# Optimization experiments

Measured on AMD Instinct MI355X. Metric: run time of the kernel, lower is better.

## Reference

```python
import jax, jax.numpy as jnp
import numpy as np

N, E, F, R, L = 20000, 320000, 128, 20, 3
CUTOFF = 5.0
EPS = 1e-15


def _p(k, shape, fan_in):
    return jax.random.normal(k, shape, dtype=jnp.float32) * (fan_in ** -0.5)


def setup_inputs() -> dict:
    key = jax.random.key(0)
    ks = jax.random.split(key, 30)
    xyz = jax.random.uniform(ks[0], (N, 3), dtype=jnp.float32, minval=0.0, maxval=12.0)
    z = jax.random.randint(ks[1], (N,), 1, 84)
    i = jax.random.randint(ks[2], (E,), 0, N)
    off = jax.random.randint(ks[3], (E,), 1, N)
    j = (i + off) % N  # guarantees i != j
    nbrs = jnp.stack([i, j], axis=1)
    return {
        'xyz': xyz, 'z': z, 'nbrs': nbrs,
        'embed': _p(ks[4], (100, F), 1),
        'msg_W1': _p(ks[5], (L, F, F), F), 'msg_b1': jnp.zeros((L, F)),
        'msg_W2': _p(ks[6], (L, F, 3 * F), F), 'msg_b2': jnp.zeros((L, 3 * F)),
        'msg_Wd': _p(ks[7], (L, R, 3 * F), R), 'msg_bd': jnp.zeros((L, 3 * F)),
        'upd_U': _p(ks[8], (L, F, F), F), 'upd_V': _p(ks[9], (L, F, F), F),
        'upd_Ws1': _p(ks[10], (L, 2 * F, F), 2 * F), 'upd_bs1': jnp.zeros((L, F)),
        'upd_Ws2': _p(ks[11], (L, F, 3 * F), F), 'upd_bs2': jnp.zeros((L, 3 * F)),
        'ro_W1': _p(ks[12], (F, F // 2), F), 'ro_b1': jnp.zeros((F // 2,)),
        'ro_W2': _p(ks[13], (F // 2, 64), F // 2), 'ro_b2': jnp.zeros((64,)),
        'fc_W1': _p(ks[14], (64, 128), 64), 'fc_b1': jnp.zeros((128,)),
        'fc_W2': _p(ks[15], (128, 128), 128), 'fc_b2': jnp.zeros((128,)),
        'fc_Wo': _p(ks[16], (128, 1), 128), 'fc_bo': jnp.zeros((1,)),
    }


def _painn_forward(xyz, z, nbrs, embed,
                   msg_W1, msg_b1, msg_W2, msg_b2, msg_Wd, msg_bd,
                   upd_U, upd_V, upd_Ws1, upd_bs1, upd_Ws2, upd_bs2,
                   ro_W1, ro_b1, ro_W2, ro_b2,
                   fc_W1, fc_b1, fc_W2, fc_b2, fc_Wo, fc_bo):
    n_atoms = xyz.shape[0]
    idx_i, idx_j = nbrs[:, 0], nbrs[:, 1]
    # neighbor displacement vectors, distances, unit vectors
    r_ij = xyz[idx_j] - xyz[idx_i]                       # [E,3]
    dist = jnp.sqrt(jnp.sum(r_ij * r_ij, -1) + EPS)      # [E]
    unit = r_ij / dist[:, None]                          # [E,3]
    # PaiNN radial basis: sin(n*pi*d/cutoff)/d, n=1..R
    n_k = jnp.arange(1, R + 1, dtype=xyz.dtype)
    rbf = jnp.sin(n_k * jnp.pi * dist[:, None] / CUTOFF) / dist[:, None]   # [E,R]
    f_cut = jnp.where(dist < CUTOFF, 0.5 * (jnp.cos(jnp.pi * dist / CUTOFF) + 1.0), 0.0)
    silu = jax.nn.silu
    s = embed[z]                                         # [N,F]
    v = jnp.zeros((n_atoms, F, 3), dtype=xyz.dtype)      # [N,F,3]
    for l in range(L):
        # --- message block ---
        phi = silu(s @ msg_W1[l] + msg_b1[l]) @ msg_W2[l] + msg_b2[l]      # [N,3F]
        w_s = (rbf @ msg_Wd[l] + msg_bd[l]) * f_cut[:, None]               # [E,3F]
        inv = (phi[idx_j] * w_s).reshape(-1, 3, F)                         # [E,3,F]
        s0, s1, s2 = inv[:, 0], inv[:, 1], inv[:, 2]
        dv_ij = s2[:, :, None] * unit[:, None, :] + s0[:, :, None] * v[idx_j]  # [E,F,3]
        ds_i = jax.ops.segment_sum(s1, idx_i, num_segments=n_atoms)
        dv_i = jax.ops.segment_sum(dv_ij, idx_i, num_segments=n_atoms)
        s = s + ds_i
        v = v + dv_i
        # --- update block ---
        u_v = jnp.einsum('nfd,fg->ngd', v, upd_U[l])
        v_v = jnp.einsum('nfd,fg->ngd', v, upd_V[l])
        v_norm = jnp.sqrt(jnp.sum(v_v * v_v, -1) + EPS)                    # [N,F]
        stack = jnp.concatenate([s, v_norm], axis=-1)                      # [N,2F]
        split = silu(stack @ upd_Ws1[l] + upd_bs1[l]) @ upd_Ws2[l] + upd_bs2[l]
        a_vv = split[:, :F, None]
        a_sv = split[:, F:2 * F]
        a_ss = split[:, 2 * F:]
        v = v + u_v * a_vv
        s = s + jnp.sum(u_v * v_v, -1) * a_sv + a_ss
    # --- readout + fully connected head (per atom) ---
    h = silu(s @ ro_W1 + ro_b1) @ ro_W2 + ro_b2                            # [N,64]
    h = jax.nn.relu(h @ fc_W1 + fc_b1)
    h = jax.nn.relu(h @ fc_W2 + fc_b2)
    return h @ fc_Wo + fc_bo                                               # [N,1]


def reference(xyz, z, nbrs, embed,
              msg_W1, msg_b1, msg_W2, msg_b2, msg_Wd, msg_bd,
              upd_U, upd_V, upd_Ws1, upd_bs1, upd_Ws2, upd_bs2,
              ro_W1, ro_b1, ro_W2, ro_b2,
              fc_W1, fc_b1, fc_W2, fc_b2, fc_Wo, fc_bo):
    return _painn_forward(xyz, z, nbrs, embed,
                          msg_W1, msg_b1, msg_W2, msg_b2, msg_Wd, msg_bd,
                          upd_U, upd_V, upd_Ws1, upd_bs1, upd_Ws2, upd_bs2,
                          ro_W1, ro_b1, ro_W2, ro_b2,
                          fc_W1, fc_b1, fc_W2, fc_b2, fc_Wo, fc_bo)
```

## Files before the change

kernel.cpp:

```cpp
#include <hip/hip_runtime.h>
#include <math.h>

static const int NA = 20000;
static const int NE = 320000;
static const int F  = 128;
static const long NF = (long)NA * F;

typedef short short8 __attribute__((ext_vector_type(8)));
typedef float f32x4  __attribute__((ext_vector_type(4)));

__global__ void geom_kernel(const float* __restrict__ xyz, const int* __restrict__ nbrs,
                            float* __restrict__ edata, int* __restrict__ act,
                            int* __restrict__ cnt) {
    int e = blockIdx.x * 256 + threadIdx.x;
    if (e >= NE) return;
    int i = nbrs[2 * e], j = nbrs[2 * e + 1];
    float xi = xyz[3 * i], yi = xyz[3 * i + 1], zi = xyz[3 * i + 2];
    float xj = xyz[3 * j], yj = xyz[3 * j + 1], zj = xyz[3 * j + 2];
    float rx = xj - xi, ry = yj - yi, rz = zj - zi;
    float d2 = rx * rx + ry * ry + rz * rz + 1e-15f;
    float d = sqrtf(d2);
    if (d >= 5.0f) { act[e] = 0; return; }
    act[e] = 1;
    atomicAdd(&cnt[i], 1);
    float inv = 1.0f / d;
    float fc = 0.5f * (cosf(d * (float)M_PI / 5.0f) + 1.0f);
    float* ed = edata + (size_t)e * 24;
    ed[0] = fc; ed[1] = rx * inv; ed[2] = ry * inv; ed[3] = rz * inv;
    float x = d * (float)M_PI / 5.0f;
    float s1 = sinf(x), c1 = cosf(x);
    float skm1 = 0.f, sk = s1;
    float twoc = 2.f * c1;
    float scale = inv * fc;
    #pragma unroll
    for (int k = 0; k < 20; k++) {
        ed[4 + k] = sk * scale;
        float skp1 = twoc * sk - skm1;
        skm1 = sk; sk = skp1;
    }
}

__global__ __launch_bounds__(1024) void scan_kernel(const int* __restrict__ cnt, int* __restrict__ offs) {
    __shared__ int sh[1024];
    const int CH = 20;
    int t = threadIdx.x;
    int base = t * CH;
    int c[CH];
    int tot = 0;
    #pragma unroll
    for (int k = 0; k < CH; k++) {
        int idx = base + k;
        c[k] = (idx < NA) ? cnt[idx] : 0;
        tot += c[k];
    }
    sh[t] = tot;
    __syncthreads();
    for (int o = 1; o < 1024; o <<= 1) {
        int v = (t >= o) ? sh[t - o] : 0;
        __syncthreads();
        sh[t] += v;
        __syncthreads();
    }
    int run = sh[t] - tot;
    #pragma unroll
    for (int k = 0; k < CH; k++) {
        int idx = base + k;
        if (idx < NA) offs[idx] = run;
        run += c[k];
    }
    if (t == 1023) offs[NA] = sh[1023];
}

__global__ void fill_kernel(const int* __restrict__ nbrs, const int* __restrict__ act,
                            const int* __restrict__ offs, int* __restrict__ cur,
                            const float* __restrict__ edata,
                            int* __restrict__ jc, float* __restrict__ edc) {
    int e = blockIdx.x * 256 + threadIdx.x;
    if (e >= NE || !act[e]) return;
    int i = nbrs[2 * e];
    int q = offs[i] + atomicAdd(&cur[i], 1);
    jc[q] = nbrs[2 * e + 1];
    const float4* src = (const float4*)(edata + (size_t)e * 24);
    float4* dst = (float4*)(edc + (size_t)q * 24);
    #pragma unroll
    for (int k = 0; k < 6; k++) dst[k] = src[k];
}

__global__ void embed_kernel(const int* __restrict__ z, const float* __restrict__ embed,
                             float* __restrict__ s, __bf16* __restrict__ sh_, __bf16* __restrict__ sl_) {
    int idx = blockIdx.x * 256 + threadIdx.x;
    if (idx >= NA * F) return;
    int n = idx >> 7, f = idx & 127;
    float v = embed[z[n] * F + f];
    s[idx] = v;
    __bf16 h = (__bf16)v;
    sh_[idx] = h; sl_[idx] = (__bf16)(v - (float)h);
}

static const int WSEG = 180224;
static const int WRO  = 3 * WSEG;
static const int WTOT = WRO + 36864;

__global__ void wconv_kernel(const float* __restrict__ W1, const float* __restrict__ W2,
                             const float* __restrict__ U, const float* __restrict__ V,
                             const float* __restrict__ Ws1, const float* __restrict__ Ws2,
                             const float* __restrict__ roW1, const float* __restrict__ roW2,
                             const float* __restrict__ fcW1, const float* __restrict__ fcW2,
                             __bf16* __restrict__ wh, __bf16* __restrict__ wl) {
    int g = blockIdx.x * 256 + threadIdx.x;
    if (g >= WTOT) return;
    const float* src; int K, N, idx;
    if (g < WRO) {
        int lay = g / WSEG, o = g - lay * WSEG;
        if (o < 16384)       { src = W1  + (size_t)lay * 16384; K = 128; N = 128; idx = o; }
        else if (o < 65536)  { src = W2  + (size_t)lay * 49152; K = 128; N = 384; idx = o - 16384; }
        else if (o < 81920)  { src = U   + (size_t)lay * 16384; K = 128; N = 128; idx = o - 65536; }
        else if (o < 98304)  { src = V   + (size_t)lay * 16384; K = 128; N = 128; idx = o - 81920; }
        else if (o < 131072) { src = Ws1 + (size_t)lay * 32768; K = 256; N = 128; idx = o - 98304; }
        else                 { src = Ws2 + (size_t)lay * 49152; K = 128; N = 384; idx = o - 131072; }
    } else {
        int o2 = g - WRO;
        if (o2 < 8192)       { src = roW1; K = 128; N = 64;  idx = o2; }
        else if (o2 < 12288) { src = roW2; K = 64;  N = 64;  idx = o2 - 8192; }
        else if (o2 < 20480) { src = fcW1; K = 64;  N = 128; idx = o2 - 12288; }
        else                 { src = fcW2; K = 128; N = 128; idx = o2 - 20480; }
    }
    int n = idx / K, k = idx - n * K;
    float v = src[(size_t)k * N + n];
    __bf16 h = (__bf16)v;
    wh[g] = h; wl[g] = (__bf16)(v - (float)h);
}

template<int ACT, int MODE>
__device__ __forceinline__ void mgemm_body(char* ldsb,
    const __bf16* __restrict__ Ah, const __bf16* __restrict__ Al,
    const __bf16* __restrict__ Bh, const __bf16* __restrict__ Bl,
    const float* __restrict__ bias, int K, int N, int c0,
    float* __restrict__ Cf, __bf16* __restrict__ Ch, __bf16* __restrict__ Cl) {
    int tid = threadIdx.x;
    int w = tid >> 6, l = tid & 63;
    int r0 = blockIdx.x * 128;

    int srow = tid >> 3, sl = tid & 7;

    int wr = w >> 2, wc = w & 3;
    int lrow = l & 15, lk = l >> 4;
    uint32_t arow[4], axor[4], brow[2], bxor[2];
    #pragma unroll
    for (int m = 0; m < 4; m++) {
        int row = wr * 64 + m * 16 + lrow;
        arow[m] = (uint32_t)row * 128u; axor[m] = (uint32_t)((row & 7) << 4);
    }
    #pragma unroll
    for (int n = 0; n < 2; n++) {
        int row = wc * 32 + n * 16 + lrow;
        brow[n] = (uint32_t)row * 128u; bxor[n] = (uint32_t)((row & 7) << 4);
    }

    f32x4 acc[4][2];
    #pragma unroll
    for (int m = 0; m < 4; m++)
        #pragma unroll
        for (int n = 0; n < 2; n++) acc[m][n] = (f32x4){0.f, 0.f, 0.f, 0.f};

    const char* pAh = (const char*)Ah;
    const char* pAl = (const char*)Al;
    const char* pBh = (const char*)Bh;
    const char* pBl = (const char*)Bl;

    for (int k0 = 0; k0 < K; k0 += 64) {
        #pragma unroll
        for (int t = 0; t < 2; t++) {
            int row = srow + t * 64;
            uint32_t dst = (uint32_t)row * 128u + (uint32_t)(((sl ^ (row & 7)) << 4));
            int ga = min(r0 + row, NA - 1);
            int gb = min(c0 + row, N - 1);
            size_t soA = ((size_t)ga * K + k0 + sl * 8) * 2;
            size_t soB = ((size_t)gb * K + k0 + sl * 8) * 2;
            *(float4*)(ldsb + dst)         = *(const float4*)(pAh + soA);
            *(float4*)(ldsb + 16384 + dst) = *(const float4*)(pAl + soA);
            *(float4*)(ldsb + 32768 + dst) = *(const float4*)(pBh + soB);
            *(float4*)(ldsb + 49152 + dst) = *(const float4*)(pBl + soB);
        }
        __syncthreads();
        #pragma unroll
        for (int kh = 0; kh < 2; kh++) {
            uint32_t ks = (uint32_t)((kh * 4 + lk) * 16);
            short8 fah[4], fal[4], fbh[2], fbl[2];
            #pragma unroll
            for (int m = 0; m < 4; m++) {
                uint32_t ob = arow[m] + (ks ^ axor[m]);
                fah[m] = *(const short8*)(ldsb + ob);
                fal[m] = *(const short8*)(ldsb + 16384 + ob);
            }
            #pragma unroll
            for (int n = 0; n < 2; n++) {
                uint32_t ob = brow[n] + (ks ^ bxor[n]);
                fbh[n] = *(const short8*)(ldsb + 32768 + ob);
                fbl[n] = *(const short8*)(ldsb + 49152 + ob);
            }
            #pragma unroll
            for (int m = 0; m < 4; m++)
                #pragma unroll
                for (int n = 0; n < 2; n++) {
                    acc[m][n] = __builtin_amdgcn_mfma_f32_16x16x32_bf16(fah[m], fbh[n], acc[m][n], 0, 0, 0);
                    acc[m][n] = __builtin_amdgcn_mfma_f32_16x16x32_bf16(fah[m], fbl[n], acc[m][n], 0, 0, 0);
                    acc[m][n] = __builtin_amdgcn_mfma_f32_16x16x32_bf16(fal[m], fbh[n], acc[m][n], 0, 0, 0);
                }
        }
        __syncthreads();
    }

    #pragma unroll
    for (int n = 0; n < 2; n++) {
        int gc = c0 + wc * 32 + n * 16 + lrow;
        float bb = (bias && gc < N) ? bias[gc] : 0.f;
        #pragma unroll
        for (int m = 0; m < 4; m++) {
            #pragma unroll
            for (int r = 0; r < 4; r++) {
                int gr = r0 + wr * 64 + m * 16 + lk * 4 + r;
                if (gr < NA && gc < N) {
                    float y = acc[m][n][r] + bb;
                    if (ACT == 1) y = y / (1.f + expf(-y));
                    if (ACT == 2) y = fmaxf(y, 0.f);
                    if (MODE == 0) {
                        Cf[(size_t)gr * N + gc] = y;
                    } else {
                        __bf16 h = (__bf16)y;
                        Ch[(size_t)gr * N + gc] = h;
                        Cl[(size_t)gr * N + gc] = (__bf16)(y - (float)h);
                    }
                }
            }
        }
    }
}

template<int ACT, int MODE>
__global__ __launch_bounds__(512, 4) void mgemm_kernel(
    const __bf16* __restrict__ Ah, const __bf16* __restrict__ Al,
    const __bf16* __restrict__ Bh, const __bf16* __restrict__ Bl,
    const float* __restrict__ bias, int K, int N,
    float* __restrict__ Cf, __bf16* __restrict__ Ch, __bf16* __restrict__ Cl) {
    __shared__ __attribute__((aligned(16))) char lds[65536];
    mgemm_body<ACT, MODE>(lds, Ah, Al, Bh, Bl, bias, K, N, blockIdx.y * 128, Cf, Ch, Cl);
}

__global__ __launch_bounds__(512, 4) void mgemm_uvvv_kernel(
    const __bf16* __restrict__ vBh, const __bf16* __restrict__ vBl,
    const __bf16* __restrict__ Uth, const __bf16* __restrict__ Utl,
    const __bf16* __restrict__ Vth, const __bf16* __restrict__ Vtl,
    float* __restrict__ uv, float* __restrict__ vv) {
    __shared__ __attribute__((aligned(16))) char lds[65536];
    int zz = blockIdx.z, d = zz % 3;
    const __bf16* Ah = vBh + (size_t)d * NF;
    const __bf16* Al = vBl + (size_t)d * NF;
    const __bf16* Bh = (zz < 3) ? Uth : Vth;
    const __bf16* Bl = (zz < 3) ? Utl : Vtl;
    float* Cf = ((zz < 3) ? uv : vv) + (size_t)d * NF;
    mgemm_body<0, 0>(lds, Ah, Al, Bh, Bl, nullptr, 128, 128, 0, Cf, nullptr, nullptr);
}

__global__ __launch_bounds__(512, 4) void mgemm_ws1_kernel(
    const __bf16* __restrict__ sh_, const __bf16* __restrict__ sl_,
    const float* __restrict__ vv,
    const __bf16* __restrict__ Bh, const __bf16* __restrict__ Bl,
    const float* __restrict__ bias,
    __bf16* __restrict__ Ch, __bf16* __restrict__ Cl) {
    __shared__ __attribute__((aligned(16))) char ldsb[65536];
    const int K = 256, N = 128;
    int tid = threadIdx.x;
    int w = tid >> 6, l = tid & 63;
    int r0 = blockIdx.x * 128;
    int srow = tid >> 3, sl = tid & 7;
    int wr = w >> 2, wc = w & 3;
    int lrow = l & 15, lk = l >> 4;
    uint32_t arow[4], axor[4], brow[2], bxor[2];
    #pragma unroll
    for (int m = 0; m < 4; m++) {
        int row = wr * 64 + m * 16 + lrow;
        arow[m] = (uint32_t)row * 128u; axor[m] = (uint32_t)((row & 7) << 4);
    }
    #pragma unroll
    for (int n = 0; n < 2; n++) {
        int row = wc * 32 + n * 16 + lrow;
        brow[n] = (uint32_t)row * 128u; bxor[n] = (uint32_t)((row & 7) << 4);
    }
    f32x4 acc[4][2];
    #pragma unroll
    for (int m = 0; m < 4; m++)
        #pragma unroll
        for (int n = 0; n < 2; n++) acc[m][n] = (f32x4){0.f, 0.f, 0.f, 0.f};

    for (int k0 = 0; k0 < K; k0 += 64) {
        #pragma unroll
        for (int t = 0; t < 2; t++) {
            int row = srow + t * 64;
            uint32_t dst = (uint32_t)row * 128u + (uint32_t)(((sl ^ (row & 7)) << 4));
            int ga = min(r0 + row, NA - 1);
            int gb = row;
            size_t soB = ((size_t)gb * K + k0 + sl * 8) * 2;
            *(float4*)(ldsb + 32768 + dst) = *(const float4*)((const char*)Bh + soB);
            *(float4*)(ldsb + 49152 + dst) = *(const float4*)((const char*)Bl + soB);
            if (k0 < 128) {
                size_t soA = ((size_t)ga * 128 + k0 + sl * 8) * 2;
                *(float4*)(ldsb + dst)         = *(const float4*)((const char*)sh_ + soA);
                *(float4*)(ldsb + 16384 + dst) = *(const float4*)((const char*)sl_ + soA);
            } else {
                int f0 = (k0 - 128) + sl * 8;
                size_t b = (size_t)ga * 128 + f0;
                float4 a0 = *(const float4*)(vv + b);
                float4 a1 = *(const float4*)(vv + b + 4);
                float4 b0 = *(const float4*)(vv + NF + b);
                float4 b1 = *(const float4*)(vv + NF + b + 4);
                float4 c0v = *(const float4*)(vv + 2 * NF + b);
                float4 c1v = *(const float4*)(vv + 2 * NF + b + 4);
                float xs[8] = {a0.x, a0.y, a0.z, a0.w, a1.x, a1.y, a1.z, a1.w};
                float ys[8] = {b0.x, b0.y, b0.z, b0.w, b1.x, b1.y, b1.z, b1.w};
                float zs[8] = {c0v.x, c0v.y, c0v.z, c0v.w, c1v.x, c1v.y, c1v.z, c1v.w};
                union { short8 s; float4 q; } hi, lo;
                #pragma unroll
                for (int k = 0; k < 8; k++) {
                    float vn = sqrtf(xs[k] * xs[k] + ys[k] * ys[k] + zs[k] * zs[k] + 1e-15f);
                    __bf16 h = (__bf16)vn;
                    hi.s[k] = *(short*)&h;
                    __bf16 lo_b = (__bf16)(vn - (float)h);
                    lo.s[k] = *(short*)&lo_b;
                }
                *(float4*)(ldsb + dst)         = hi.q;
                *(float4*)(ldsb + 16384 + dst) = lo.q;
            }
        }
        __syncthreads();
        #pragma unroll
        for (int kh = 0; kh < 2; kh++) {
            uint32_t ks = (uint32_t)((kh * 4 + lk) * 16);
            short8 fah[4], fal[4], fbh[2], fbl[2];
            #pragma unroll
            for (int m = 0; m < 4; m++) {
                uint32_t ob = arow[m] + (ks ^ axor[m]);
                fah[m] = *(const short8*)(ldsb + ob);
                fal[m] = *(const short8*)(ldsb + 16384 + ob);
            }
            #pragma unroll
            for (int n = 0; n < 2; n++) {
                uint32_t ob = brow[n] + (ks ^ bxor[n]);
                fbh[n] = *(const short8*)(ldsb + 32768 + ob);
                fbl[n] = *(const short8*)(ldsb + 49152 + ob);
            }
            #pragma unroll
            for (int m = 0; m < 4; m++)
                #pragma unroll
                for (int n = 0; n < 2; n++) {
                    acc[m][n] = __builtin_amdgcn_mfma_f32_16x16x32_bf16(fah[m], fbh[n], acc[m][n], 0, 0, 0);
                    acc[m][n] = __builtin_amdgcn_mfma_f32_16x16x32_bf16(fah[m], fbl[n], acc[m][n], 0, 0, 0);
                    acc[m][n] = __builtin_amdgcn_mfma_f32_16x16x32_bf16(fal[m], fbh[n], acc[m][n], 0, 0, 0);
                }
        }
        __syncthreads();
    }
    #pragma unroll
    for (int n = 0; n < 2; n++) {
        int gc = wc * 32 + n * 16 + lrow;
        float bb = bias[gc];
        #pragma unroll
        for (int m = 0; m < 4; m++) {
            #pragma unroll
            for (int r = 0; r < 4; r++) {
                int gr = r0 + wr * 64 + m * 16 + lk * 4 + r;
                if (gr < NA) {
                    float y = acc[m][n][r] + bb;
                    y = y / (1.f + expf(-y));
                    __bf16 h = (__bf16)y;
                    Ch[(size_t)gr * N + gc] = h;
                    Cl[(size_t)gr * N + gc] = (__bf16)(y - (float)h);
                }
            }
        }
    }
}

__global__ __launch_bounds__(128) void msg_kernel(
    const float* __restrict__ phi, const float* __restrict__ edc,
    const int* __restrict__ jc, const int* __restrict__ offs,
    const float* __restrict__ Wd, const float* __restrict__ bd,
    const float* __restrict__ vin, float* __restrict__ s,
    __bf16* __restrict__ sh_, __bf16* __restrict__ sl_,
    __bf16* __restrict__ vBh, __bf16* __restrict__ vBl) {
    int i = blockIdx.x;
    int f = threadIdx.x;
    float wd0[20], wd1[20], wd2[20];
    #pragma unroll
    for (int k = 0; k < 20; k++) {
        wd0[k] = Wd[k * 384 + f];
        wd1[k] = Wd[k * 384 + 128 + f];
        wd2[k] = Wd[k * 384 + 256 + f];
    }
    float b0 = bd[f], b1 = bd[128 + f], b2 = bd[256 + f];
    float accS = 0.f, aV0 = 0.f, aV1 = 0.f, aV2 = 0.f;
    int p0 = offs[i], p1 = offs[i + 1];
    for (int p = p0; p < p1; ++p) {
        int j = jc[p];
        const float4* ed = (const float4*)(edc + (size_t)p * 24);
        float4 q0 = ed[0], q1 = ed[1], q2 = ed[2], q3 = ed[3], q4 = ed[4], q5 = ed[5];
        float fc = q0.x, ux = q0.y, uy = q0.z, uz = q0.w;
        float rb[20];
        rb[0]=q1.x; rb[1]=q1.y; rb[2]=q1.z; rb[3]=q1.w;
        rb[4]=q2.x; rb[5]=q2.y; rb[6]=q2.z; rb[7]=q2.w;
        rb[8]=q3.x; rb[9]=q3.y; rb[10]=q3.z; rb[11]=q3.w;
        rb[12]=q4.x; rb[13]=q4.y; rb[14]=q4.z; rb[15]=q4.w;
        rb[16]=q5.x; rb[17]=q5.y; rb[18]=q5.z; rb[19]=q5.w;
        float w0 = b0 * fc, w1 = b1 * fc, w2 = b2 * fc;
        #pragma unroll
        for (int k = 0; k < 20; k++) {
            w0 += rb[k] * wd0[k];
            w1 += rb[k] * wd1[k];
            w2 += rb[k] * wd2[k];
        }
        const float* pj = phi + (size_t)j * 384;
        float i0 = pj[f] * w0, i1 = pj[128 + f] * w1, i2 = pj[256 + f] * w2;
        const float* vj = vin + (size_t)j * 384;
        accS += i1;
        aV0 += i2 * ux + i0 * vj[f];
        aV1 += i2 * uy + i0 * vj[128 + f];
        aV2 += i2 * uz + i0 * vj[256 + f];
    }
    size_t ib = (size_t)i * F + f;
    float ns = s[ib] + accS;
    s[ib] = ns;
    __bf16 hs = (__bf16)ns;
    sh_[ib] = hs; sl_[ib] = (__bf16)(ns - (float)hs);
    const float* vi = vin + (size_t)i * 384;
    float o0 = vi[f] + aV0;
    float o1 = vi[128 + f] + aV1;
    float o2 = vi[256 + f] + aV2;
    __bf16 h0 = (__bf16)o0, h1 = (__bf16)o1, h2 = (__bf16)o2;
    vBh[ib] = h0;            vBl[ib] = (__bf16)(o0 - (float)h0);
    vBh[NF + ib] = h1;       vBl[NF + ib] = (__bf16)(o1 - (float)h1);
    vBh[2 * NF + ib] = h2;   vBl[2 * NF + ib] = (__bf16)(o2 - (float)h2);
}

__global__ void update_kernel(const float* __restrict__ spl, const float* __restrict__ uv,
                              const float* __restrict__ vv,
                              const __bf16* __restrict__ vBh, const __bf16* __restrict__ vBl,
                              float* __restrict__ vout, float* __restrict__ s,
                              __bf16* __restrict__ sh_, __bf16* __restrict__ sl_) {
    int idx = blockIdx.x * 256 + threadIdx.x;
    if (idx >= NA * F) return;
    int n = idx >> 7, f = idx & 127;
    const float* sp = spl + (size_t)n * 384;
    float avv = sp[f], asv = sp[128 + f], ass = sp[256 + f];
    float dot = 0.f;
    #pragma unroll
    for (int d = 0; d < 3; d++) {
        float u = uv[d * NF + idx];
        float vb = (float)vBh[d * NF + idx] + (float)vBl[d * NF + idx];
        vout[(size_t)n * 384 + d * 128 + f] = vb + u * avv;
        dot += u * vv[d * NF + idx];
    }
    float ns = s[idx] + dot * asv + ass;
    s[idx] = ns;
    __bf16 h = (__bf16)ns;
    sh_[idx] = h; sl_[idx] = (__bf16)(ns - (float)h);
}

__global__ __launch_bounds__(256) void head_kernel(const float* __restrict__ h,
                                                   const float* __restrict__ Wo,
                                                   const float* __restrict__ bo,
                                                   float* __restrict__ out) {
    int n = blockIdx.x * 4 + (threadIdx.x >> 6);
    int lane = threadIdx.x & 63;
    if (n >= NA) return;
    float p = h[(size_t)n * 128 + lane] * Wo[lane] + h[(size_t)n * 128 + 64 + lane] * Wo[64 + lane];
    #pragma unroll
    for (int o = 32; o > 0; o >>= 1) p += __shfl_down(p, o);
    if (lane == 0) out[n] = p + bo[0];
}

extern "C" void kernel_launch(void* const* d_in, const int* in_sizes, int n_in,
                              void* d_out, int out_size, void* d_ws, size_t ws_size,
                              hipStream_t stream) {
    const float* xyz    = (const float*)d_in[0];
    const int*   z      = (const int*)d_in[1];
    const int*   nbrs   = (const int*)d_in[2];
    const float* embed  = (const float*)d_in[3];
    const float* msg_W1 = (const float*)d_in[4];
    const float* msg_b1 = (const float*)d_in[5];
    const float* msg_W2 = (const float*)d_in[6];
    const float* msg_b2 = (const float*)d_in[7];
    const float* msg_Wd = (const float*)d_in[8];
    const float* msg_bd = (const float*)d_in[9];
    const float* upd_U  = (const float*)d_in[10];
    const float* upd_V  = (const float*)d_in[11];
    const float* upd_Ws1= (const float*)d_in[12];
    const float* upd_bs1= (const float*)d_in[13];
    const float* upd_Ws2= (const float*)d_in[14];
    const float* upd_bs2= (const float*)d_in[15];
    const float* ro_W1  = (const float*)d_in[16];
    const float* ro_b1  = (const float*)d_in[17];
    const float* ro_W2  = (const float*)d_in[18];
    const float* ro_b2  = (const float*)d_in[19];
    const float* fc_W1  = (const float*)d_in[20];
    const float* fc_b1  = (const float*)d_in[21];
    const float* fc_W2  = (const float*)d_in[22];
    const float* fc_b2  = (const float*)d_in[23];
    const float* fc_Wo  = (const float*)d_in[24];
    const float* fc_bo  = (const float*)d_in[25];
    float* out = (float*)d_out;

    char* ws = (char*)d_ws;
    size_t off = 0;
    auto alloc = [&](size_t nbytes) -> char* {
        char* p = ws + off;
        off += (nbytes + 255) / 256 * 256;
        return p;
    };
    float*  edc   = (float*)alloc((size_t)NE * 24 * 4);
    float*  s     = (float*)alloc((size_t)NA * F * 4);
    __bf16* sh_   = (__bf16*)alloc((size_t)NA * F * 2);
    __bf16* sl_   = (__bf16*)alloc((size_t)NA * F * 2);
    float*  vA    = (float*)alloc((size_t)3 * NF * 4);
    __bf16* vBh   = (__bf16*)alloc((size_t)3 * NF * 2);
    __bf16* vBl   = (__bf16*)alloc((size_t)3 * NF * 2);
    float*  phi   = (float*)alloc((size_t)NA * 384 * 4);
    __bf16* hid_h = (__bf16*)alloc((size_t)NA * F * 2);
    __bf16* hid_l = (__bf16*)alloc((size_t)NA * F * 2);
    float*  uv    = (float*)alloc((size_t)3 * NF * 4);
    float*  vv    = (float*)alloc((size_t)3 * NF * 4);
    __bf16* stkh  = (__bf16*)alloc((size_t)NA * 256 * 2);
    __bf16* stkl  = (__bf16*)alloc((size_t)NA * 256 * 2);
    __bf16* wt_h  = (__bf16*)alloc((size_t)WTOT * 2);
    __bf16* wt_l  = (__bf16*)alloc((size_t)WTOT * 2);
    int* act  = (int*)alloc((size_t)NE * 4);
    int* cnt2 = (int*)alloc((size_t)2 * NA * 4);
    int* offs = (int*)alloc((size_t)(NA + 1) * 4);
    int* jc   = (int*)alloc((size_t)NE * 4);
    int* cnt = cnt2;
    int* cur = cnt2 + NA;

    float* edata = uv;
    __bf16* t1h = hid_h, *t1l = hid_l;
    __bf16* t2h = stkh,  *t2l = stkl;
    __bf16* t3h = sh_,   *t3l = sl_;
    float*  t4  = phi;

    hipMemsetAsync(cnt2, 0, (size_t)2 * NA * 4, stream);
    geom_kernel<<<(NE + 255) / 256, 256, 0, stream>>>(xyz, nbrs, edata, act, cnt);
    scan_kernel<<<1, 1024, 0, stream>>>(cnt, offs);
    fill_kernel<<<(NE + 255) / 256, 256, 0, stream>>>(nbrs, act, offs, cur, edata, jc, edc);

    wconv_kernel<<<(WTOT + 255) / 256, 256, 0, stream>>>(msg_W1, msg_W2, upd_U, upd_V,
                                                         upd_Ws1, upd_Ws2, ro_W1, ro_W2,
                                                         fc_W1, fc_W2, wt_h, wt_l);
    hipMemsetAsync(vA, 0, (size_t)3 * NF * 4, stream);
    embed_kernel<<<(NA * F + 255) / 256, 256, 0, stream>>>(z, embed, s, sh_, sl_);

    const int GX = (NA + 127) / 128;
    const int EW = (NA * F + 255) / 256;
    for (int l = 0; l < 3; l++) {
        const __bf16* w1h = wt_h + (size_t)l * WSEG,          *w1l = wt_l + (size_t)l * WSEG;
        const __bf16* w2h = w1h + 16384,  *w2l = w1l + 16384;
        const __bf16* uh  = w1h + 65536,  *ul  = w1l + 65536;
        const __bf16* vh  = w1h + 81920,  *vl  = w1l + 81920;
        const __bf16* s1h = w1h + 98304,  *s1l = w1l + 98304;
        const __bf16* s2h = w1h + 131072, *s2l = w1l + 131072;

        mgemm_kernel<1, 1><<<dim3(GX, 1), 512, 0, stream>>>(sh_, sl_, w1h, w1l,
            msg_b1 + (size_t)l * 128, 128, 128, nullptr, hid_h, hid_l);
        mgemm_kernel<0, 0><<<dim3(GX, 3), 512, 0, stream>>>(hid_h, hid_l, w2h, w2l,
            msg_b2 + (size_t)l * 384, 128, 384, phi, nullptr, nullptr);
        msg_kernel<<<NA, 128, 0, stream>>>(phi, edc, jc, offs,
            msg_Wd + (size_t)l * 20 * 384, msg_bd + (size_t)l * 384,
            vA, s, sh_, sl_, vBh, vBl);
        mgemm_uvvv_kernel<<<dim3(GX, 1, 6), 512, 0, stream>>>(vBh, vBl, uh, ul, vh, vl, uv, vv);
        mgemm_ws1_kernel<<<dim3(GX, 1), 512, 0, stream>>>(sh_, sl_, vv, s1h, s1l,
            upd_bs1 + (size_t)l * 128, hid_h, hid_l);
        mgemm_kernel<0, 0><<<dim3(GX, 3), 512, 0, stream>>>(hid_h, hid_l, s2h, s2l,
            upd_bs2 + (size_t)l * 384, 128, 384, phi, nullptr, nullptr);
        update_kernel<<<EW, 256, 0, stream>>>(phi, uv, vv, vBh, vBl, vA, s, sh_, sl_);
    }

    const __bf16* roh = wt_h + WRO, *rol = wt_l + WRO;
    mgemm_kernel<1, 1><<<dim3(GX, 1), 512, 0, stream>>>(sh_, sl_, roh, rol,
        ro_b1, 128, 64, nullptr, t1h, t1l);
    mgemm_kernel<0, 1><<<dim3(GX, 1), 512, 0, stream>>>(t1h, t1l, roh + 8192, rol + 8192,
        ro_b2, 64, 64, nullptr, t2h, t2l);
    mgemm_kernel<2, 1><<<dim3(GX, 1), 512, 0, stream>>>(t2h, t2l, roh + 12288, rol + 12288,
        fc_b1, 64, 128, nullptr, t3h, t3l);
    mgemm_kernel<2, 0><<<dim3(GX, 1), 512, 0, stream>>>(t3h, t3l, roh + 20480, rol + 20480,
        fc_b2, 128, 128, t4, nullptr, nullptr);
    head_kernel<<<NA / 4, 256, 0, stream>>>(t4, fc_Wo, fc_bo, out);
}
```

Baseline: 601.2 us.

## Fuse per-atom update elementwise step into the following GEMM's A-tile load

Removes the standalone update_kernel and computes the vector/scalar update while staging the A operand of the next layer's message W1 GEMM, or of the readout's first GEMM after the last layer. The updated s is split into bf16 hi/lo directly into LDS, and v and s are written back to global memory only when needed. This avoids a separate launch and a round trip of s through bf16 buffers. In exchange, the GEMM prologue carries heavier global loads, which could lengthen its latency.

```diff
diff --git a/kernel.cpp b/kernel.cpp
--- a/kernel.cpp
+++ b/kernel.cpp
@@ -7,6 +7,7 @@
 static const long NF = (long)NA * F;
 
 typedef short short8 __attribute__((ext_vector_type(8)));
+typedef __bf16 bf16x8 __attribute__((ext_vector_type(8)));
 typedef float f32x4  __attribute__((ext_vector_type(4)));
 
 __global__ void geom_kernel(const float* __restrict__ xyz, const int* __restrict__ nbrs,
@@ -381,6 +382,157 @@
     }
 }
 
+template<int NOUT, int WRST>
+__global__ __launch_bounds__(512, 4) void mgemm_upd_kernel(
+    const float* __restrict__ spl, const float* __restrict__ uv, const float* __restrict__ vv,
+    const __bf16* __restrict__ vBh, const __bf16* __restrict__ vBl,
+    const __bf16* __restrict__ Bh, const __bf16* __restrict__ Bl,
+    const float* __restrict__ bias,
+    float* __restrict__ vA, float* __restrict__ sBuf,
+    __bf16* __restrict__ Ch, __bf16* __restrict__ Cl) {
+    __shared__ __attribute__((aligned(16))) char ldsb[65536];
+    const int K = 128;
+    int tid = threadIdx.x;
+    int w = tid >> 6, l = tid & 63;
+    int r0 = blockIdx.x * 128;
+    int srow = tid >> 3, sl = tid & 7;
+    int wr = w >> 2, wc = w & 3;
+    int lrow = l & 15, lk = l >> 4;
+    uint32_t arow[4], axor[4], brow[2], bxor[2];
+    #pragma unroll
+    for (int m = 0; m < 4; m++) {
+        int row = wr * 64 + m * 16 + lrow;
+        arow[m] = (uint32_t)row * 128u; axor[m] = (uint32_t)((row & 7) << 4);
+    }
+    #pragma unroll
+    for (int n = 0; n < 2; n++) {
+        int row = wc * 32 + n * 16 + lrow;
+        brow[n] = (uint32_t)row * 128u; bxor[n] = (uint32_t)((row & 7) << 4);
+    }
+    f32x4 acc[4][2];
+    #pragma unroll
+    for (int m = 0; m < 4; m++)
+        #pragma unroll
+        for (int n = 0; n < 2; n++) acc[m][n] = (f32x4){0.f, 0.f, 0.f, 0.f};
+
+    for (int k0 = 0; k0 < K; k0 += 64) {
+        #pragma unroll
+        for (int t = 0; t < 2; t++) {
+            int row = srow + t * 64;
+            uint32_t dst = (uint32_t)row * 128u + (uint32_t)(((sl ^ (row & 7)) << 4));
+            int gr0 = r0 + row;
+            bool real = gr0 < NA;
+            int ga = real ? gr0 : (NA - 1);
+            int gb = min(row, NOUT - 1);
+            size_t soB = ((size_t)gb * K + k0 + sl * 8) * 2;
+            *(float4*)(ldsb + 32768 + dst) = *(const float4*)((const char*)Bh + soB);
+            *(float4*)(ldsb + 49152 + dst) = *(const float4*)((const char*)Bl + soB);
+
+            int f0 = k0 + sl * 8;
+            const float* sp = spl + (size_t)ga * 384;
+            float4 av0 = *(const float4*)(sp + f0);
+            float4 av1 = *(const float4*)(sp + f0 + 4);
+            float avv[8] = {av0.x, av0.y, av0.z, av0.w, av1.x, av1.y, av1.z, av1.w};
+            float dot[8] = {0.f, 0.f, 0.f, 0.f, 0.f, 0.f, 0.f, 0.f};
+            size_t eb = (size_t)ga * 128 + f0;
+            #pragma unroll
+            for (int d = 0; d < 3; d++) {
+                float4 u0 = *(const float4*)(uv + d * NF + eb);
+                float4 u1 = *(const float4*)(uv + d * NF + eb + 4);
+                float4 w0 = *(const float4*)(vv + d * NF + eb);
+                float4 w1 = *(const float4*)(vv + d * NF + eb + 4);
+                bf16x8 bh = *(const bf16x8*)(vBh + d * NF + eb);
+                bf16x8 bl = *(const bf16x8*)(vBl + d * NF + eb);
+                float uu[8] = {u0.x, u0.y, u0.z, u0.w, u1.x, u1.y, u1.z, u1.w};
+                float ww[8] = {w0.x, w0.y, w0.z, w0.w, w1.x, w1.y, w1.z, w1.w};
+                float nv[8];
+                #pragma unroll
+                for (int k = 0; k < 8; k++) {
+                    float vb = (float)bh[k] + (float)bl[k];
+                    nv[k] = vb + uu[k] * avv[k];
+                    dot[k] += uu[k] * ww[k];
+                }
+                if (WRST && real) {
+                    float* vp = vA + (size_t)ga * 384 + d * 128 + f0;
+                    *(float4*)(vp)     = make_float4(nv[0], nv[1], nv[2], nv[3]);
+                    *(float4*)(vp + 4) = make_float4(nv[4], nv[5], nv[6], nv[7]);
+                }
+            }
+            float4 as0 = *(const float4*)(sp + 128 + f0);
+            float4 as1 = *(const float4*)(sp + 128 + f0 + 4);
+            float4 az0 = *(const float4*)(sp + 256 + f0);
+            float4 az1 = *(const float4*)(sp + 256 + f0 + 4);
+            float4 sv0 = *(const float4*)(sBuf + eb);
+            float4 sv1 = *(const float4*)(sBuf + eb + 4);
+            float asv[8] = {as0.x, as0.y, as0.z, as0.w, as1.x, as1.y, as1.z, as1.w};
+            float ass[8] = {az0.x, az0.y, az0.z, az0.w, az1.x, az1.y, az1.z, az1.w};
+            float sv[8]  = {sv0.x, sv0.y, sv0.z, sv0.w, sv1.x, sv1.y, sv1.z, sv1.w};
+            float ns[8];
+            union { short8 s; float4 q; } hi, lo;
+            #pragma unroll
+            for (int k = 0; k < 8; k++) {
+                ns[k] = sv[k] + dot[k] * asv[k] + ass[k];
+                __bf16 h = (__bf16)ns[k];
+                hi.s[k] = *(short*)&h;
+                __bf16 lo_b = (__bf16)(ns[k] - (float)h);
+                lo.s[k] = *(short*)&lo_b;
+            }
+            if (WRST && real) {
+                *(float4*)(sBuf + eb)     = make_float4(ns[0], ns[1], ns[2], ns[3]);
+                *(float4*)(sBuf + eb + 4) = make_float4(ns[4], ns[5], ns[6], ns[7]);
+            }
+            *(float4*)(ldsb + dst)         = hi.q;
+            *(float4*)(ldsb + 16384 + dst) = lo.q;
+        }
+        __syncthreads();
+        #pragma unroll
+        for (int kh = 0; kh < 2; kh++) {
+            uint32_t ks = (uint32_t)((kh * 4 + lk) * 16);
+            short8 fah[4], fal[4], fbh[2], fbl[2];
+            #pragma unroll
+            for (int m = 0; m < 4; m++) {
+                uint32_t ob = arow[m] + (ks ^ axor[m]);
+                fah[m] = *(const short8*)(ldsb + ob);
+                fal[m] = *(const short8*)(ldsb + 16384 + ob);
+            }
+            #pragma unroll
+            for (int n = 0; n < 2; n++) {
+                uint32_t ob = brow[n] + (ks ^ bxor[n]);
+                fbh[n] = *(const short8*)(ldsb + 32768 + ob);
+                fbl[n] = *(const short8*)(ldsb + 49152 + ob);
+            }
+            #pragma unroll
+            for (int m = 0; m < 4; m++)
+                #pragma unroll
+                for (int n = 0; n < 2; n++) {
+                    acc[m][n] = __builtin_amdgcn_mfma_f32_16x16x32_bf16(fah[m], fbh[n], acc[m][n], 0, 0, 0);
+                    acc[m][n] = __builtin_amdgcn_mfma_f32_16x16x32_bf16(fah[m], fbl[n], acc[m][n], 0, 0, 0);
+                    acc[m][n] = __builtin_amdgcn_mfma_f32_16x16x32_bf16(fal[m], fbh[n], acc[m][n], 0, 0, 0);
+                }
+        }
+        __syncthreads();
+    }
+    #pragma unroll
+    for (int n = 0; n < 2; n++) {
+        int gc = wc * 32 + n * 16 + lrow;
+        float bb = (gc < NOUT) ? bias[gc] : 0.f;
+        #pragma unroll
+        for (int m = 0; m < 4; m++) {
+            #pragma unroll
+            for (int r = 0; r < 4; r++) {
+                int gr = r0 + wr * 64 + m * 16 + lk * 4 + r;
+                if (gr < NA && gc < NOUT) {
+                    float y = acc[m][n][r] + bb;
+                    y = y / (1.f + expf(-y));
+                    __bf16 h = (__bf16)y;
+                    Ch[(size_t)gr * NOUT + gc] = h;
+                    Cl[(size_t)gr * NOUT + gc] = (__bf16)(y - (float)h);
+                }
+            }
+        }
+    }
+}
+
 __global__ __launch_bounds__(128) void msg_kernel(
     const float* __restrict__ phi, const float* __restrict__ edc,
     const int* __restrict__ jc, const int* __restrict__ offs,
@@ -439,30 +591,6 @@
     vBh[ib] = h0;            vBl[ib] = (__bf16)(o0 - (float)h0);
     vBh[NF + ib] = h1;       vBl[NF + ib] = (__bf16)(o1 - (float)h1);
     vBh[2 * NF + ib] = h2;   vBl[2 * NF + ib] = (__bf16)(o2 - (float)h2);
-}
-
-__global__ void update_kernel(const float* __restrict__ spl, const float* __restrict__ uv,
-                              const float* __restrict__ vv,
-                              const __bf16* __restrict__ vBh, const __bf16* __restrict__ vBl,
-                              float* __restrict__ vout, float* __restrict__ s,
-                              __bf16* __restrict__ sh_, __bf16* __restrict__ sl_) {
-    int idx = blockIdx.x * 256 + threadIdx.x;
-    if (idx >= NA * F) return;
-    int n = idx >> 7, f = idx & 127;
-    const float* sp = spl + (size_t)n * 384;
-    float avv = sp[f], asv = sp[128 + f], ass = sp[256 + f];
-    float dot = 0.f;
-    #pragma unroll
-    for (int d = 0; d < 3; d++) {
-        float u = uv[d * NF + idx];
-        float vb = (float)vBh[d * NF + idx] + (float)vBl[d * NF + idx];
-        vout[(size_t)n * 384 + d * 128 + f] = vb + u * avv;
-        dot += u * vv[d * NF + idx];
-    }
-    float ns = s[idx] + dot * asv + ass;
-    s[idx] = ns;
-    __bf16 h = (__bf16)ns;
-    sh_[idx] = h; sl_[idx] = (__bf16)(ns - (float)h);
 }
 
 __global__ __launch_bounds__(256) void head_kernel(const float* __restrict__ h,
@@ -557,7 +685,6 @@
     embed_kernel<<<(NA * F + 255) / 256, 256, 0, stream>>>(z, embed, s, sh_, sl_);
 
     const int GX = (NA + 127) / 128;
-    const int EW = (NA * F + 255) / 256;
     for (int l = 0; l < 3; l++) {
         const __bf16* w1h = wt_h + (size_t)l * WSEG,          *w1l = wt_l + (size_t)l * WSEG;
         const __bf16* w2h = w1h + 16384,  *w2l = w1l + 16384;
@@ -566,8 +693,14 @@
         const __bf16* s1h = w1h + 98304,  *s1l = w1l + 98304;
         const __bf16* s2h = w1h + 131072, *s2l = w1l + 131072;
 
-        mgemm_kernel<1, 1><<<dim3(GX, 1), 512, 0, stream>>>(sh_, sl_, w1h, w1l,
-            msg_b1 + (size_t)l * 128, 128, 128, nullptr, hid_h, hid_l);
+        if (l == 0) {
+            mgemm_kernel<1, 1><<<dim3(GX, 1), 512, 0, stream>>>(sh_, sl_, w1h, w1l,
+                msg_b1 + (size_t)l * 128, 128, 128, nullptr, hid_h, hid_l);
+        } else {
+            mgemm_upd_kernel<128, 1><<<dim3(GX, 1), 512, 0, stream>>>(
+                phi, uv, vv, vBh, vBl, w1h, w1l, msg_b1 + (size_t)l * 128,
+                vA, s, hid_h, hid_l);
+        }
         mgemm_kernel<0, 0><<<dim3(GX, 3), 512, 0, stream>>>(hid_h, hid_l, w2h, w2l,
             msg_b2 + (size_t)l * 384, 128, 384, phi, nullptr, nullptr);
         msg_kernel<<<NA, 128, 0, stream>>>(phi, edc, jc, offs,
@@ -578,12 +711,11 @@
             upd_bs1 + (size_t)l * 128, hid_h, hid_l);
         mgemm_kernel<0, 0><<<dim3(GX, 3), 512, 0, stream>>>(hid_h, hid_l, s2h, s2l,
             upd_bs2 + (size_t)l * 384, 128, 384, phi, nullptr, nullptr);
-        update_kernel<<<EW, 256, 0, stream>>>(phi, uv, vv, vBh, vBl, vA, s, sh_, sl_);
     }
 
     const __bf16* roh = wt_h + WRO, *rol = wt_l + WRO;
-    mgemm_kernel<1, 1><<<dim3(GX, 1), 512, 0, stream>>>(sh_, sl_, roh, rol,
-        ro_b1, 128, 64, nullptr, t1h, t1l);
+    mgemm_upd_kernel<64, 0><<<dim3(GX, 1), 512, 0, stream>>>(
+        phi, uv, vv, vBh, vBl, roh, rol, ro_b1, nullptr, s, t1h, t1l);
     mgemm_kernel<0, 1><<<dim3(GX, 1), 512, 0, stream>>>(t1h, t1l, roh + 8192, rol + 8192,
         ro_b2, 64, 64, nullptr, t2h, t2l);
     mgemm_kernel<2, 1><<<dim3(GX, 1), 512, 0, stream>>>(t2h, t2l, roh + 12288, rol + 12288,
```

Measured after the change: 578.7 us, median of 2. 1.04x faster.
